# Kernel optimization log

Measured on AMD Instinct MI355X. Metric: run time of the kernel, lower is better.

## Reference

```python
import jax, jax.numpy as jnp
import numpy as np

REGION_RADIUS = 5
REGION_SIZE = 2 * REGION_RADIUS + 1  # 11
VOCAB = 50000
EMB = 128
B, L = 32, 512


def setup_inputs() -> dict:
    key = jax.random.key(0)
    k1, k2, k3 = jax.random.split(key, 3)
    seq = jax.random.randint(k1, (B, L, 1), 0, VOCAB, dtype=jnp.int64)
    W = jax.random.normal(k2, (VOCAB, EMB), dtype=jnp.float32)
    U = jax.random.normal(k3, (VOCAB * REGION_SIZE, EMB), dtype=jnp.float32)
    return {"seq": seq, "W": W, "U": U}


def reference(seq, W, U):
    # seq: [B, L, 1] int token ids
    r = REGION_RADIUS
    padded = jnp.pad(seq, ((0, 0), (r, r), (0, 0)))  # [B, L+2r, 1]
    L_ = seq.shape[1]
    # sliding-window gather: win_idx[l, j] = l + j
    win_idx = jnp.arange(L_)[:, None] + jnp.arange(REGION_SIZE)[None, :]  # [L, R]
    windows = padded[:, win_idx, :]                      # [B, L, R, 1]
    windows = jnp.transpose(windows, (0, 1, 3, 2))       # [B, L, 1, R]
    # align index: token_id * region_size + window offset (the _bias)
    align_idx = windows * REGION_SIZE + jnp.arange(REGION_SIZE)  # [B, L, 1, R]
    align_emb = U[align_idx]                             # [B, L, 1, R, E]
    trigram_emb = W[seq][..., None, :]                   # [B, L, 1, 1, E]
    projected = align_emb * trigram_emb                  # [B, L, 1, R, E]
    mask = (seq != 0).astype(jnp.float32)[..., None]     # [B, L, 1, 1]
    h = jnp.max(projected, axis=-2) * mask               # [B, L, 1, E]
    return h
```

## Files before the change

### kernel.cpp

```cpp
#include <hip/hip_runtime.h>

#define BB 32
#define LL 512
#define EMB 128
#define RS 11
#define RR 5

typedef float f4 __attribute__((ext_vector_type(4)));

__global__ __launch_bounds__(256) void region_encoder_kernel(
    const int* __restrict__ seq,
    const float* __restrict__ W,
    const float* __restrict__ U,
    float* __restrict__ out)
{
    const int row0 = blockIdx.x * 8;
    const int b    = row0 >> 9;
    const int l0   = row0 & 511;

    __shared__ int toks[RS + 8 - 1];
    if (threadIdx.x < RS + 8 - 1) {
        const int p = l0 - RR + (int)threadIdx.x;
        toks[threadIdx.x] = (p >= 0 && p < LL) ? seq[(b << 9) + p] : 0;
    }
    __syncthreads();

    const int r    = threadIdx.x >> 5;
    const int lane = threadIdx.x & 31;
    const int row  = row0 + r;

    const int s = toks[r + RR];

    const f4* W4 = (const f4*)(W + (size_t)s * EMB);
    const f4  t  = W4[lane];

    f4 m = (f4){-INFINITY, -INFINITY, -INFINITY, -INFINITY};

    #pragma unroll
    for (int j = 0; j < RS; ++j) {
        const int w = toks[r + j];
        const f4* U4 = (const f4*)(U + (size_t)(w * RS + j) * EMB);
        const f4 u = U4[lane];
        m.x = fmaxf(m.x, u.x * t.x);
        m.y = fmaxf(m.y, u.y * t.y);
        m.z = fmaxf(m.z, u.z * t.z);
        m.w = fmaxf(m.w, u.w * t.w);
    }

    f4 res;
    if (s != 0) {
        res = m;
    } else {
        res = (f4){0.f, 0.f, 0.f, 0.f};
    }
    __builtin_nontemporal_store(res, (f4*)(out + (size_t)row * EMB) + lane);
}

extern "C" void kernel_launch(void* const* d_in, const int* in_sizes, int n_in,
                              void* d_out, int out_size, void* d_ws, size_t ws_size,
                              hipStream_t stream)
{
    const int*   seq = (const int*)  d_in[0];
    const float* W   = (const float*)d_in[1];
    const float* U   = (const float*)d_in[2];
    float* out = (float*)d_out;

    const int rows = BB * LL;
    const int blocks = rows / 8;
    region_encoder_kernel<<<blocks, 256, 0, stream>>>(seq, W, U, out);
}
```

Before: 343.9 us.

## Gather contiguous per-token U blocks and accumulate window max in LDS tile

Each block now handles 64 output rows instead of 8. For every token slot in the window it loads all 11 consecutive U rows (one contiguous 5.6 KB block) rather than 11 scattered 512-byte rows per output. Contributions are scattered into a shared-memory max tile, one window offset at a time, with W rows staged in shared memory. The aim is to turn random row gathers into contiguous streaming reads, with fewer TLB and DRAM page misses. The cost is many barriers, LDS read-modify-write traffic, high register use and only 256 blocks, which may leave latency exposed.

After: 360.5 us. 4.8% more time.

```diff
diff --git a/kernel.cpp b/kernel.cpp
--- a/kernel.cpp
+++ b/kernel.cpp
@@ -5,6 +5,9 @@
 #define EMB 128
 #define RS 11
 #define RR 5
+#define NR 64
+#define NSLOT (NR + RS - 1)
+#define NSLOTP 80
 
 typedef float f4 __attribute__((ext_vector_type(4)));
 
@@ -14,46 +17,92 @@
     const float* __restrict__ U,
     float* __restrict__ out)
 {
-    const int row0 = blockIdx.x * 8;
+    __shared__ float tile[NR * EMB];
+    __shared__ float wt  [NR * EMB];
+    __shared__ int   toks[NSLOTP];
+
+    const int tid  = threadIdx.x;
+    const int wv   = tid >> 6;
+    const int lane = tid & 63;
+    const int hw   = tid >> 5;
+    const int hl   = tid & 31;
+
+    const int row0 = blockIdx.x * NR;
     const int b    = row0 >> 9;
     const int l0   = row0 & 511;
+    const int* seqb = seq + (b << 9);
 
-    __shared__ int toks[RS + 8 - 1];
-    if (threadIdx.x < RS + 8 - 1) {
-        const int p = l0 - RR + (int)threadIdx.x;
-        toks[threadIdx.x] = (p >= 0 && p < LL) ? seq[(b << 9) + p] : 0;
+    if (tid < NSLOTP) {
+        const int p = l0 - RR + tid;
+        toks[tid] = (tid < NSLOT && p >= 0 && p < LL) ? seqb[p] : 0;
     }
     __syncthreads();
 
-    const int r    = threadIdx.x >> 5;
-    const int lane = threadIdx.x & 31;
-    const int row  = row0 + r;
-
-    const int s = toks[r + RR];
-
-    const f4* W4 = (const f4*)(W + (size_t)s * EMB);
-    const f4  t  = W4[lane];
-
-    f4 m = (f4){-INFINITY, -INFINITY, -INFINITY, -INFINITY};
+    f4* tile4 = (f4*)tile;
+    f4* wt4   = (f4*)wt;
 
     #pragma unroll
-    for (int j = 0; j < RS; ++j) {
-        const int w = toks[r + j];
-        const f4* U4 = (const f4*)(U + (size_t)(w * RS + j) * EMB);
-        const f4 u = U4[lane];
-        m.x = fmaxf(m.x, u.x * t.x);
-        m.y = fmaxf(m.y, u.y * t.y);
-        m.z = fmaxf(m.z, u.z * t.z);
-        m.w = fmaxf(m.w, u.w * t.w);
+    for (int rr = 0; rr < 8; ++rr) {
+        const int r   = rr * 8 + hw;
+        const int tok = toks[r + RR];
+        wt4[r * 32 + hl] = ((const f4*)(W + (size_t)tok * EMB))[hl];
+    }
+    #pragma unroll
+    for (int k = 0; k < 8; ++k)
+        tile4[k * 256 + tid] = (f4){-INFINITY, -INFINITY, -INFINITY, -INFINITY};
+    __syncthreads();
+
+    const f4* U4 = (const f4*)U;
+    const int s0w = wv * 20;
+
+    for (int t = 0; t < 5; ++t) {
+        const int s0 = s0w + t * 4;
+
+        f4 u[4][6];
+        #pragma unroll
+        for (int c = 0; c < 4; ++c) {
+            const int slot = s0 + c;
+            if (slot < NSLOT) {
+                const size_t base = (size_t)toks[slot] * (RS * 32);
+                #pragma unroll
+                for (int k = 0; k < 5; ++k)
+                    u[c][k] = U4[base + (size_t)(k * 64 + lane)];
+                if (lane < 32)
+                    u[c][5] = U4[base + (size_t)(320 + lane)];
+            }
+        }
+
+        #pragma unroll
+        for (int j = 0; j < RS; ++j) {
+            __syncthreads();
+            const int k = j >> 1;
+            const int h = j & 1;
+            #pragma unroll
+            for (int c = 0; c < 4; ++c) {
+                const int r_out = s0 + c - j;
+                if (r_out >= 0 && r_out < NR && (lane >> 5) == h) {
+                    const f4 uv = u[c][k];
+                    const f4 tv = wt4[r_out * 32 + hl];
+                    f4 cur = tile4[r_out * 32 + hl];
+                    cur.x = fmaxf(cur.x, uv.x * tv.x);
+                    cur.y = fmaxf(cur.y, uv.y * tv.y);
+                    cur.z = fmaxf(cur.z, uv.z * tv.z);
+                    cur.w = fmaxf(cur.w, uv.w * tv.w);
+                    tile4[r_out * 32 + hl] = cur;
+                }
+            }
+        }
     }
 
-    f4 res;
-    if (s != 0) {
-        res = m;
-    } else {
-        res = (f4){0.f, 0.f, 0.f, 0.f};
+    __syncthreads();
+    #pragma unroll
+    for (int rr = 0; rr < 8; ++rr) {
+        const int r = rr * 8 + hw;
+        const int s = toks[r + RR];
+        f4 v = tile4[r * 32 + hl];
+        if (s == 0) v = (f4){0.f, 0.f, 0.f, 0.f};
+        __builtin_nontemporal_store(v, (f4*)(out + (size_t)(row0 + r) * EMB) + hl);
     }
-    __builtin_nontemporal_store(res, (f4*)(out + (size_t)row * EMB) + lane);
 }
 
 extern "C" void kernel_launch(void* const* d_in, const int* in_sizes, int n_in,
@@ -65,7 +114,7 @@
     const float* U   = (const float*)d_in[2];
     float* out = (float*)d_out;
 
-    const int rows = BB * LL;
-    const int blocks = rows / 8;
+    const int rows   = BB * LL;
+    const int blocks = rows / NR;
     region_encoder_kernel<<<blocks, 256, 0, stream>>>(seq, W, U, out);
 }
```
